# Performance work log

Measured on AMD Instinct MI355X. Metric: run time of the kernel, lower is better.

## Reference

```python
import jax, jax.numpy as jnp
import numpy as np

B, IN, OUT, G = 64, 8192, 8192, 64
NG = IN // G  # groups per row


def setup_inputs() -> dict:
    key = jax.random.key(0)
    k1, k2, k3, k4 = jax.random.split(key, 4)
    x = jax.random.normal(k1, (B, IN), dtype=jnp.float32)
    # packed 2-bit codes: 4 codes per byte, LSB-first (matches _pack2)
    w_packed = jax.random.randint(k2, (OUT, IN // 4), 0, 256, dtype=jnp.int32).astype(jnp.uint8)
    # scales from _calc_group_qparams are positive (max_abs/1.5); zp is always 2
    scales = jax.random.uniform(k3, (OUT, NG), dtype=jnp.float32, minval=0.01, maxval=0.1)
    zps = jnp.full((OUT, NG), 2, dtype=jnp.int32)
    bias = jax.random.normal(k4, (OUT,), dtype=jnp.float32) * 0.01
    return {"x": x, "w_packed": w_packed, "scales": scales, "zps": zps, "bias": bias}


def _dequant(w_packed, scales, zps):
    # unpack: byte -> 4 two-bit codes, LSB first (matches _unpack2)
    out_f = w_packed.shape[0]
    codes = jnp.stack([(w_packed >> s) & 3 for s in (0, 2, 4, 6)], axis=-1)  # [OUT, IN//4, 4]
    q = codes.reshape(out_f, NG, G).astype(jnp.int32)                        # [OUT, NG, G]
    # per-group dequant: (q - zp) * scale
    w = (q - zps[:, :, None]).astype(jnp.float32) * scales[:, :, None]
    return w.reshape(out_f, IN)                                              # [OUT, IN]


def reference(x, w_packed, scales, zps, bias):
    w = _dequant(w_packed, scales, zps)  # [OUT, IN] fp32
    # original accumulates xg @ wg.T per group; equivalent to full x @ w.T
    return x @ w.T + bias                # [B, OUT]
```

## Files before the change

### kernel.cpp

```cpp
#include <hip/hip_runtime.h>
#include <hip/hip_bf16.h>

#define B_    64
#define IN_   8192
#define OUT_  8192
#define NG_   128
#define PB_   2048

#define KSPLIT 16
#define KC     512
#define KSTEPS 16

typedef float f32x4 __attribute__((ext_vector_type(4)));
typedef short s16x8 __attribute__((ext_vector_type(8)));

union U16 {
    uint4 u4;
    s16x8 s8;
    unsigned int w[4];
};

__global__ __launch_bounds__(256) void k_flag_init(int* flag) {
    if (threadIdx.x == 0 && blockIdx.x == 0) *flag = 1;
}

__global__ __launch_bounds__(256) void k_detect(const unsigned int* __restrict__ w,
                                                int* __restrict__ flag) {
    unsigned v = w[blockIdx.x * 256 + threadIdx.x];
    if (v > 255u) *flag = 0;
}

__global__ __launch_bounds__(256) void k_cvt(const float* __restrict__ x,
                                             __hip_bfloat16* __restrict__ xb) {
    int i = (blockIdx.x * 256 + threadIdx.x) * 4;
    const float4 f = *(const float4*)(x + i);
    __hip_bfloat162 h0 = __float22bfloat162_rn(make_float2(f.x, f.y));
    __hip_bfloat162 h1 = __float22bfloat162_rn(make_float2(f.z, f.w));
    uint2 o;
    o.x = *(unsigned int*)&h0;
    o.y = *(unsigned int*)&h1;
    *(uint2*)(xb + i) = o;
}

__global__ __launch_bounds__(256) void k_bias(const float* __restrict__ bias,
                                              float* __restrict__ out) {
    int i = (blockIdx.x * 256 + threadIdx.x) * 4;
    int n = i & (OUT_ - 1);
    *(float4*)(out + i) = *(const float4*)(bias + n);
}

__global__ __launch_bounds__(512, 4) void k_main(
    const __hip_bfloat16* __restrict__ xb,
    const unsigned char* __restrict__ wp,
    const float* __restrict__ scales,
    const int* __restrict__ zps,
    float* __restrict__ out,
    const int* __restrict__ flag)
{
    __shared__ uint4 lds[4096];

    const int tid   = threadIdx.x;
    const int bid   = blockIdx.x;
    const int nblk  = bid & 63;
    const int kidx  = bid >> 6;
    const int kbase = kidx * KC;

#pragma unroll
    for (int it = 0; it < 8; ++it) {
        int slot = tid + it * 512;
        int lane = slot & 63;
        int mt   = (slot >> 6) & 3;
        int kb   = slot >> 8;
        int qq   = lane >> 4, rr = lane & 15;
        int row  = mt * 16 + rr;
        int kk   = kbase + kb * 32 + qq * 8;
        lds[slot] = *(const uint4*)(xb + row * IN_ + kk);
    }
    __syncthreads();

    const int wave = tid >> 6;
    const int lane = tid & 63;
    const int q    = lane >> 4, nn = lane & 15;
    const int n    = nblk * 128 + wave * 16 + nn;

    const bool i32mode = (*flag != 0);

    f32x4 acc0 = {0.f, 0.f, 0.f, 0.f};
    f32x4 acc1 = acc0, acc2 = acc0, acc3 = acc0;

    const int wbase = n * PB_ + (kbase >> 2) + q * 2;
    const float* srow = scales + n * NG_;
    const int*   zrow = zps + n * NG_;

#pragma unroll 4
    for (int kb = 0; kb < KSTEPS; ++kb) {
        unsigned u;
        if (i32mode) {
            const int2 two = *(const int2*)((const int*)wp + wbase + kb * 8);
            u = (unsigned)(two.x & 0xFF) | ((unsigned)(two.y & 0xFF) << 8);
        } else {
            u = *(const unsigned short*)(wp + wbase + kb * 8);
        }
        const int   ng = (kbase + kb * 32) >> 6;
        const float s  = srow[ng];
        const int   zp = zrow[ng];

        U16 bf;
#pragma unroll
        for (int jj = 0; jj < 4; ++jj) {
            float a0 = (float)((int)((u >> (4 * jj)) & 3u) - zp) * s;
            float a1 = (float)((int)((u >> (4 * jj + 2)) & 3u) - zp) * s;
            __hip_bfloat162 h = __float22bfloat162_rn(make_float2(a0, a1));
            bf.w[jj] = *(unsigned int*)&h;
        }

        U16 a0v, a1v, a2v, a3v;
        a0v.u4 = lds[(kb * 4 + 0) * 64 + lane];
        a1v.u4 = lds[(kb * 4 + 1) * 64 + lane];
        a2v.u4 = lds[(kb * 4 + 2) * 64 + lane];
        a3v.u4 = lds[(kb * 4 + 3) * 64 + lane];
        acc0 = __builtin_amdgcn_mfma_f32_16x16x32_bf16(a0v.s8, bf.s8, acc0, 0, 0, 0);
        acc1 = __builtin_amdgcn_mfma_f32_16x16x32_bf16(a1v.s8, bf.s8, acc1, 0, 0, 0);
        acc2 = __builtin_amdgcn_mfma_f32_16x16x32_bf16(a2v.s8, bf.s8, acc2, 0, 0, 0);
        acc3 = __builtin_amdgcn_mfma_f32_16x16x32_bf16(a3v.s8, bf.s8, acc3, 0, 0, 0);
    }

#pragma unroll
    for (int r = 0; r < 4; ++r) {
        atomicAdd(out + (0 * 16 + q * 4 + r) * OUT_ + n, acc0[r]);
        atomicAdd(out + (1 * 16 + q * 4 + r) * OUT_ + n, acc1[r]);
        atomicAdd(out + (2 * 16 + q * 4 + r) * OUT_ + n, acc2[r]);
        atomicAdd(out + (3 * 16 + q * 4 + r) * OUT_ + n, acc3[r]);
    }
}

extern "C" void kernel_launch(void* const* d_in, const int* in_sizes, int n_in,
                              void* d_out, int out_size, void* d_ws, size_t ws_size,
                              hipStream_t stream) {
    const float*         x      = (const float*)d_in[0];
    const unsigned char* wp     = (const unsigned char*)d_in[1];
    const float*         scales = (const float*)d_in[2];
    const int*           zps    = (const int*)d_in[3];
    const float*         bias   = (const float*)d_in[4];
    float*               out    = (float*)d_out;

    __hip_bfloat16* xb   = (__hip_bfloat16*)d_ws;
    int*            flag = (int*)((char*)d_ws + (1 << 20));

    k_flag_init<<<1, 256, 0, stream>>>(flag);
    k_detect<<<16, 256, 0, stream>>>((const unsigned int*)wp, flag);
    k_cvt<<<(B_ * IN_ / 4) / 256, 256, 0, stream>>>(x, xb);
    k_bias<<<(B_ * OUT_ / 4) / 256, 256, 0, stream>>>(bias, out);
    k_main<<<64 * KSPLIT, 512, 0, stream>>>(xb, wp, scales, zps, out, flag);
}
```

Before: 161.1 us.

## Restructure dequant-GEMM with wider column tiles, async LDS loads, and fused prep kernels

Merges the flag-init, detect, convert and bias kernels into one prep kernel and moves the weight-format and zero-point detection into the main kernel's prologue. Each wave now covers 64 output columns (four 16-column groups) instead of 16, so every x fragment read from LDS feeds four MFMAs. All weight bytes are loaded up front. The x tile is staged with global_load_lds, and dequant is a single fma plus a byte-permute truncation to bf16. Scales are multiplied by a small fudge factor, presumably to offset the bias of truncation versus round-to-nearest. This trades numerical behaviour and extra register pressure for fewer launches and more reuse.

```diff
diff --git a/kernel.cpp b/kernel.cpp
--- a/kernel.cpp
+++ b/kernel.cpp
@@ -9,128 +9,163 @@
 
 #define KSPLIT 16
 #define KC     512
-#define KSTEPS 16
+#define CGS    4
 
 typedef float f32x4 __attribute__((ext_vector_type(4)));
 typedef short s16x8 __attribute__((ext_vector_type(8)));
 
-union U16 {
-    uint4 u4;
-    s16x8 s8;
-    unsigned int w[4];
-};
+union FU { float f; unsigned u; };
 
-__global__ __launch_bounds__(256) void k_flag_init(int* flag) {
-    if (threadIdx.x == 0 && blockIdx.x == 0) *flag = 1;
+__global__ __launch_bounds__(256) void k_pre(const float* __restrict__ x,
+                                             const float* __restrict__ bias,
+                                             __hip_bfloat16* __restrict__ xb,
+                                             float* __restrict__ out) {
+    const int bid = blockIdx.x;
+    if (bid < 512) {
+        int i = (bid * 256 + threadIdx.x) * 4;
+        float4 f = *(const float4*)(x + i);
+        __hip_bfloat162 h0 = __float22bfloat162_rn(make_float2(f.x, f.y));
+        __hip_bfloat162 h1 = __float22bfloat162_rn(make_float2(f.z, f.w));
+        uint2 o; o.x = *(unsigned*)&h0; o.y = *(unsigned*)&h1;
+        *(uint2*)(xb + i) = o;
+    } else {
+        int i = ((bid - 512) * 256 + threadIdx.x) * 4;
+        *(float4*)(out + i) = *(const float4*)(bias + (i & (OUT_ - 1)));
+    }
 }
 
-__global__ __launch_bounds__(256) void k_detect(const unsigned int* __restrict__ w,
-                                                int* __restrict__ flag) {
-    unsigned v = w[blockIdx.x * 256 + threadIdx.x];
-    if (v > 255u) *flag = 0;
-}
-
-__global__ __launch_bounds__(256) void k_cvt(const float* __restrict__ x,
-                                             __hip_bfloat16* __restrict__ xb) {
-    int i = (blockIdx.x * 256 + threadIdx.x) * 4;
-    const float4 f = *(const float4*)(x + i);
-    __hip_bfloat162 h0 = __float22bfloat162_rn(make_float2(f.x, f.y));
-    __hip_bfloat162 h1 = __float22bfloat162_rn(make_float2(f.z, f.w));
-    uint2 o;
-    o.x = *(unsigned int*)&h0;
-    o.y = *(unsigned int*)&h1;
-    *(uint2*)(xb + i) = o;
-}
-
-__global__ __launch_bounds__(256) void k_bias(const float* __restrict__ bias,
-                                              float* __restrict__ out) {
-    int i = (blockIdx.x * 256 + threadIdx.x) * 4;
-    int n = i & (OUT_ - 1);
-    *(float4*)(out + i) = *(const float4*)(bias + n);
-}
-
-__global__ __launch_bounds__(512, 4) void k_main(
+__global__ __launch_bounds__(256, 2) void k_main(
     const __hip_bfloat16* __restrict__ xb,
     const unsigned char* __restrict__ wp,
     const float* __restrict__ scales,
     const int* __restrict__ zps,
-    float* __restrict__ out,
-    const int* __restrict__ flag)
+    float* __restrict__ out)
 {
-    __shared__ uint4 lds[4096];
+    __shared__ uint4 x_lds[4096];
+    __shared__ int wflag, zflag;
 
-    const int tid   = threadIdx.x;
-    const int bid   = blockIdx.x;
-    const int nblk  = bid & 63;
-    const int kidx  = bid >> 6;
-    const int kbase = kidx * KC;
+    const int tid  = threadIdx.x;
+    const int wave = tid >> 6;
+    const int lane = tid & 63;
+    const int q    = lane >> 4;
+    const int nn   = lane & 15;
+
+    const int bid     = blockIdx.x;
+    const int kidx    = bid & (KSPLIT - 1);
+    const int nblk    = bid >> 4;
+    const int kbase   = kidx * KC;
+    const int colbase = nblk * 256 + wave * 64;
 
 #pragma unroll
-    for (int it = 0; it < 8; ++it) {
-        int slot = tid + it * 512;
-        int lane = slot & 63;
-        int mt   = (slot >> 6) & 3;
-        int kb   = slot >> 8;
-        int qq   = lane >> 4, rr = lane & 15;
-        int row  = mt * 16 + rr;
-        int kk   = kbase + kb * 32 + qq * 8;
-        lds[slot] = *(const uint4*)(xb + row * IN_ + kk);
+    for (int i = 0; i < 16; ++i) {
+        int sg = wave * 16 + i;
+        int sb = sg >> 4, b = (sg >> 2) & 3, mt = sg & 3;
+        const __hip_bfloat16* src =
+            xb + (mt * 16 + nn) * IN_ + kbase + sb * 128 + q * 32 + b * 8;
+        unsigned int* dst = (unsigned int*)((char*)x_lds + sg * 1024);
+        __builtin_amdgcn_global_load_lds(
+            (const __attribute__((address_space(1))) unsigned int*)src,
+            (__attribute__((address_space(3))) unsigned int*)dst, 16, 0, 0);
     }
+
+    unsigned wv = ((const unsigned int*)wp)[tid];
+    int      zv = zps[tid];
+    if (tid == 0) { wflag = 0; zflag = 0; }
     __syncthreads();
+    if (wv > 255u) wflag = 1;
+    if (zv != 2)   zflag = 1;
+    __syncthreads();
+    const bool u8mode = (wflag != 0);
+    const bool zgen   = (zflag != 0);
 
-    const int wave = tid >> 6;
-    const int lane = tid & 63;
-    const int q    = lane >> 4, nn = lane & 15;
-    const int n    = nblk * 128 + wave * 16 + nn;
+    uint2 w8[4][CGS];
+    const int wb = (kbase >> 2) + q * 8;
+    if (u8mode) {
+#pragma unroll
+        for (int sb = 0; sb < 4; ++sb)
+#pragma unroll
+            for (int cg = 0; cg < CGS; ++cg) {
+                int n = colbase + cg * 16 + nn;
+                w8[sb][cg] = *(const uint2*)(wp + n * PB_ + wb + sb * 32);
+            }
+    } else {
+        const int* wpi = (const int*)wp;
+#pragma unroll
+        for (int sb = 0; sb < 4; ++sb)
+#pragma unroll
+            for (int cg = 0; cg < CGS; ++cg) {
+                int n = colbase + cg * 16 + nn;
+                const int* p = wpi + n * PB_ + wb + sb * 32;
+                uint4 a  = *(const uint4*)p;
+                uint4 b2 = *(const uint4*)(p + 4);
+                w8[sb][cg].x = __builtin_amdgcn_perm(a.y,  a.x,  0x0C0C0400) |
+                               __builtin_amdgcn_perm(a.w,  a.z,  0x04000C0C);
+                w8[sb][cg].y = __builtin_amdgcn_perm(b2.y, b2.x, 0x0C0C0400) |
+                               __builtin_amdgcn_perm(b2.w, b2.z, 0x04000C0C);
+            }
+    }
 
-    const bool i32mode = (*flag != 0);
-
-    f32x4 acc0 = {0.f, 0.f, 0.f, 0.f};
-    f32x4 acc1 = acc0, acc2 = acc0, acc3 = acc0;
-
-    const int wbase = n * PB_ + (kbase >> 2) + q * 2;
-    const float* srow = scales + n * NG_;
-    const int*   zrow = zps + n * NG_;
-
-#pragma unroll 4
-    for (int kb = 0; kb < KSTEPS; ++kb) {
-        unsigned u;
-        if (i32mode) {
-            const int2 two = *(const int2*)((const int*)wp + wbase + kb * 8);
-            u = (unsigned)(two.x & 0xFF) | ((unsigned)(two.y & 0xFF) << 8);
-        } else {
-            u = *(const unsigned short*)(wp + wbase + kb * 8);
-        }
-        const int   ng = (kbase + kb * 32) >> 6;
-        const float s  = srow[ng];
-        const int   zp = zrow[ng];
-
-        U16 bf;
+    float sf[4][CGS], fb[4][CGS];
 #pragma unroll
-        for (int jj = 0; jj < 4; ++jj) {
-            float a0 = (float)((int)((u >> (4 * jj)) & 3u) - zp) * s;
-            float a1 = (float)((int)((u >> (4 * jj + 2)) & 3u) - zp) * s;
-            __hip_bfloat162 h = __float22bfloat162_rn(make_float2(a0, a1));
-            bf.w[jj] = *(unsigned int*)&h;
+    for (int sb = 0; sb < 4; ++sb)
+#pragma unroll
+        for (int cg = 0; cg < CGS; ++cg) {
+            int n = colbase + cg * 16 + nn;
+            int g = kidx * 8 + sb * 2 + (q >> 1);
+            float s = scales[n * NG_ + g] * 1.001953125f;
+            float zpf = zgen ? (float)zps[n * NG_ + g] : 2.0f;
+            sf[sb][cg] = s;
+            fb[sb][cg] = -zpf * s;
         }
 
-        U16 a0v, a1v, a2v, a3v;
-        a0v.u4 = lds[(kb * 4 + 0) * 64 + lane];
-        a1v.u4 = lds[(kb * 4 + 1) * 64 + lane];
-        a2v.u4 = lds[(kb * 4 + 2) * 64 + lane];
-        a3v.u4 = lds[(kb * 4 + 3) * 64 + lane];
-        acc0 = __builtin_amdgcn_mfma_f32_16x16x32_bf16(a0v.s8, bf.s8, acc0, 0, 0, 0);
-        acc1 = __builtin_amdgcn_mfma_f32_16x16x32_bf16(a1v.s8, bf.s8, acc1, 0, 0, 0);
-        acc2 = __builtin_amdgcn_mfma_f32_16x16x32_bf16(a2v.s8, bf.s8, acc2, 0, 0, 0);
-        acc3 = __builtin_amdgcn_mfma_f32_16x16x32_bf16(a3v.s8, bf.s8, acc3, 0, 0, 0);
+    f32x4 acc[CGS][4];
+#pragma unroll
+    for (int cg = 0; cg < CGS; ++cg)
+#pragma unroll
+        for (int mt = 0; mt < 4; ++mt)
+            acc[cg][mt] = (f32x4){0.f, 0.f, 0.f, 0.f};
+
+#pragma unroll
+    for (int sb = 0; sb < 4; ++sb) {
+#pragma unroll
+        for (int dw = 0; dw < 2; ++dw) {
+#pragma unroll
+            for (int h = 0; h < 2; ++h) {
+                const int b = dw * 2 + h;
+                union { uint4 u4; s16x8 s8; } av[4];
+#pragma unroll
+                for (int mt = 0; mt < 4; ++mt)
+                    av[mt].u4 = x_lds[((sb * 4 + b) * 4 + mt) * 64 + lane];
+#pragma unroll
+                for (int cg = 0; cg < CGS; ++cg) {
+                    const unsigned v = dw ? w8[sb][cg].y : w8[sb][cg].x;
+                    const float s = sf[sb][cg], fbv = fb[sb][cg];
+                    union { unsigned u[4]; s16x8 s8; } bf;
+#pragma unroll
+                    for (int m = 0; m < 4; ++m) {
+                        const int sh = h * 16 + m * 4;
+                        FU f0, f1;
+                        f0.f = fmaf((float)((v >> sh) & 3u), s, fbv);
+                        f1.f = fmaf((float)((v >> (sh + 2)) & 3u), s, fbv);
+                        bf.u[m] = __builtin_amdgcn_perm(f1.u, f0.u, 0x07060302);
+                    }
+#pragma unroll
+                    for (int mt = 0; mt < 4; ++mt)
+                        acc[cg][mt] = __builtin_amdgcn_mfma_f32_16x16x32_bf16(
+                            av[mt].s8, bf.s8, acc[cg][mt], 0, 0, 0);
+                }
+            }
+        }
     }
 
 #pragma unroll
-    for (int r = 0; r < 4; ++r) {
-        atomicAdd(out + (0 * 16 + q * 4 + r) * OUT_ + n, acc0[r]);
-        atomicAdd(out + (1 * 16 + q * 4 + r) * OUT_ + n, acc1[r]);
-        atomicAdd(out + (2 * 16 + q * 4 + r) * OUT_ + n, acc2[r]);
-        atomicAdd(out + (3 * 16 + q * 4 + r) * OUT_ + n, acc3[r]);
+    for (int cg = 0; cg < CGS; ++cg) {
+        const int col = colbase + cg * 16 + nn;
+#pragma unroll
+        for (int mt = 0; mt < 4; ++mt)
+#pragma unroll
+            for (int r = 0; r < 4; ++r)
+                atomicAdd(out + (mt * 16 + q * 4 + r) * OUT_ + col, acc[cg][mt][r]);
     }
 }
 
@@ -144,12 +179,8 @@
     const float*         bias   = (const float*)d_in[4];
     float*               out    = (float*)d_out;
 
-    __hip_bfloat16* xb   = (__hip_bfloat16*)d_ws;
-    int*            flag = (int*)((char*)d_ws + (1 << 20));
+    __hip_bfloat16* xb = (__hip_bfloat16*)d_ws;
 
-    k_flag_init<<<1, 256, 0, stream>>>(flag);
-    k_detect<<<16, 256, 0, stream>>>((const unsigned int*)wp, flag);
-    k_cvt<<<(B_ * IN_ / 4) / 256, 256, 0, stream>>>(x, xb);
-    k_bias<<<(B_ * OUT_ / 4) / 256, 256, 0, stream>>>(bias, out);
-    k_main<<<64 * KSPLIT, 512, 0, stream>>>(xb, wp, scales, zps, out, flag);
+    k_pre<<<1024, 256, 0, stream>>>(x, bias, xb, out);
+    k_main<<<512, 256, 0, stream>>>(xb, wp, scales, zps, out);
 }
```

New measurement: 133.5 us. 1.21x faster.
